# Kernel optimization log

Measured on AMD Instinct MI355X. Metric: run time of the kernel, lower is better.

## Reference

```python
import jax, jax.numpy as jnp
import numpy as np

B, D = 64, 1024
TAU = 1.0
NEG_SLOPE = 0.01  # torch LeakyReLU default


def setup_inputs() -> dict:
    key = jax.random.key(0)
    ks = jax.random.split(key, 7)
    lim = 1.0 / np.sqrt(D)
    return {
        "x": jax.random.normal(ks[0], (B, D), dtype=jnp.float32),
        "W1": jax.random.uniform(ks[1], (D, D), jnp.float32, -lim, lim),
        "b1": jax.random.uniform(ks[2], (D,), jnp.float32, -lim, lim),
        "W2": jax.random.uniform(ks[3], (D, D), jnp.float32, -lim, lim),
        "b2": jax.random.uniform(ks[4], (D,), jnp.float32, -lim, lim),
        "W3": jax.random.uniform(ks[5], (2, D), jnp.float32, -lim, lim),
        "b3": jax.random.uniform(ks[6], (2,), jnp.float32, -lim, lim),
    }


def _leaky(h):
    return jnp.where(h >= 0, h, NEG_SLOPE * h)


def _neural_sort(scores):
    # scores: [B, D]
    d = scores.shape[1]
    s = scores[..., None]                                  # [B, D, 1]
    A = jnp.abs(s - jnp.swapaxes(s, 1, 2))                 # [B, D, D] pairwise |s_i - s_j|
    # A @ (ones @ ones^T) == row-sum of A broadcast over columns
    Bsum = jnp.sum(A, axis=-1, keepdims=True)              # [B, D, 1]
    scaling = (d - 1 - 2 * jnp.arange(d)).astype(scores.dtype)  # (d+1-2*(i+1))
    C = s * scaling[None, None, :]                         # [B, D, D]
    P_max = jnp.swapaxes(C - Bsum, 1, 2)                   # [B, D, D]
    return jax.nn.softmax(P_max / TAU, axis=-1)


def reference(x, W1, b1, W2, b2, W3, b3):
    P_hat = _neural_sort(x)                                # [B, D, D]
    xs = jnp.einsum("bij,bj->bi", P_hat, x)                # soft-sorted x
    h = _leaky(xs @ W1.T + b1)
    h = _leaky(h @ W2.T + b2)
    return h @ W3.T + b3                                   # [B, 2]
```

## Files before the change

kernel.cpp:

```cpp
#include <hip/hip_runtime.h>
#include <math.h>

constexpr int Bn = 64;
constexpr int Dn = 1024;
constexpr float LOG2E = 1.4426950408889634f;
constexpr float LN2   = 0.6931471805599453f;

__device__ __forceinline__ float exp2_fast(float v) {
#if defined(__has_builtin)
#if __has_builtin(__builtin_amdgcn_exp2f)
  return __builtin_amdgcn_exp2f(v);
#else
  return exp2f(v);
#endif
#else
  return exp2f(v);
#endif
}

__global__ __launch_bounds__(512) void k0_sort_bsum(
    const float* __restrict__ x, float2* __restrict__ pairs_s,
    float4* __restrict__ desc, float* __restrict__ out) {
  int b    = blockIdx.x >> 1;
  int half = blockIdx.x & 1;
  int tid = threadIdx.x;
  __shared__ float xs_[Dn];
  __shared__ float cs_[Dn];
  __shared__ int   bkt_[Dn];
  __shared__ int   cnt[64], base_[64], off_[64];
  __shared__ float Ssum[64], cN[64], cS[64];
  if (tid < 64) { cnt[tid] = 0; off_[tid] = 0; Ssum[tid] = 0.f; }
  __syncthreads();
  float2 v2 = *(const float2*)(x + b * Dn + tid * 2);
  float xv[2] = {v2.x, v2.y};
  int bk[2];
#pragma unroll
  for (int u = 0; u < 2; ++u) {
    float z = exp2_fast(-2.455532f * xv[u]);
    float p = 1.f / (1.f + z);
    int t = (int)(p * 64.f);
    bk[u] = t < 0 ? 0 : (t > 63 ? 63 : t);
    atomicAdd(&cnt[bk[u]], 1);
    atomicAdd(&Ssum[bk[u]], xv[u]);
  }
  __syncthreads();
  if (tid < 64) {
    int c = cnt[tid]; int si = c;
    float fs = Ssum[tid]; float ss = fs;
#pragma unroll
    for (int d = 1; d < 64; d <<= 1) {
      int oi = __shfl_up(si, d, 64);
      float os = __shfl_up(ss, d, 64);
      if (tid >= d) { si += oi; ss += os; }
    }
    base_[tid] = si - c;
    float Stot = __shfl(ss, 63, 64);
    float Slo = ss - fs;
    cN[tid] = (float)(2 * (si - c) + c - Dn);
    cS[tid] = Stot - 2.f * Slo - fs;
  }
  __syncthreads();
#pragma unroll
  for (int u = 0; u < 2; ++u) {
    int pos = base_[bk[u]] + atomicAdd(&off_[bk[u]], 1);
    xs_[pos] = xv[u];
    bkt_[pos] = bk[u];
  }
  __syncthreads();
  {
    int p = half * 512 + tid;
    float xp = xs_[p];
    int q = bkt_[p];
    int lo = base_[q], hi = lo + cnt[q];
    float local = 0.f;
    for (int k = lo; k < hi; ++k) local += fabsf(xp - xs_[k]);
    float Bs = fmaf(xp, cN[q], cS[q]) + local;
    float c = -Bs * LOG2E;
    cs_[p] = c;
    pairs_s[b * Dn + p] = make_float2(xp * LOG2E, c);
  }
  __syncthreads();
  if (tid < 64) {
    int g = half * 64 + tid;
    int base = g * 8;
    float xlo = xs_[base], xhi = xlo;
    int ilo = base, ihi = base;
#pragma unroll
    for (int k = 1; k < 8; ++k) {
      float xx = xs_[base + k];
      if (xx < xlo) { xlo = xx; ilo = base + k; }
      if (xx > xhi) { xhi = xx; ihi = base + k; }
    }
    desc[b * 128 + g] =
        make_float4(xlo * LOG2E, cs_[ilo], xhi * LOG2E, cs_[ihi]);
  }
  if (b == 0 && half == 0 && tid < 128) out[tid] = 0.f;
}

__global__ __launch_bounds__(256, 4) void k2_softsort(
    const float2* __restrict__ pairs_s, const float4* __restrict__ desc,
    float* __restrict__ xs_out) {
  __shared__ float redM[4][64], redE[4][64], redD[4][64];
  int b  = blockIdx.x >> 4;
  int rc = blockIdx.x & 15;
  int tid = threadIdx.x;
  int w = tid >> 6, lane = tid & 63;
  int i = rc * 64 + lane;
  float sc = (float)(Dn - 1 - 2 * i);
  const float2* ps = pairs_s + b * Dn;
  const float4* dp = desc + b * 128;

  float gm[32];
  float m = -3.4e38f;
#pragma unroll 8
  for (int q = 0; q < 32; ++q) {
    float4 d = dp[q * 4 + w];
    float t0 = fmaf(sc, d.x, d.y);
    float t1 = fmaf(sc, d.z, d.w);
    float g = fmaxf(t0, t1);
    gm[q] = g;
    m = fmaxf(m, g);
  }
  redM[w][lane] = m;
  __syncthreads();
  float M = fmaxf(fmaxf(redM[0][lane], redM[1][lane]),
                  fmaxf(redM[2][lane], redM[3][lane]));
  float thresh = M - 32.f;

  float se = 0.f, sd = 0.f;
#pragma unroll 4
  for (int q = 0; q < 32; ++q) {
    if (__any(gm[q] > thresh)) {
      int base = (q * 4 + w) * 8;
#pragma unroll
      for (int u = 0; u < 8; ++u) {
        float2 v = ps[base + u];
        float e = exp2_fast(fmaf(sc, v.x, v.y - M));
        se += e;
        sd = fmaf(e, v.x, sd);
      }
    }
  }
  redE[w][lane] = se;
  redD[w][lane] = sd;
  __syncthreads();
  if (tid < 64) {
    float SE = (redE[0][lane] + redE[1][lane]) + (redE[2][lane] + redE[3][lane]);
    float SD = (redD[0][lane] + redD[1][lane]) + (redD[2][lane] + redD[3][lane]);
    xs_out[b * Dn + rc * 64 + lane] = SD / SE * LN2;
  }
}

template <bool TAIL>
__global__ __launch_bounds__(256) void layer_kernel(
    const float* __restrict__ in, const float* __restrict__ W,
    const float* __restrict__ bias, float* __restrict__ out,
    const float* __restrict__ W3, const float* __restrict__ b3,
    float* __restrict__ out2) {
  __shared__ float s[8][Dn + 4];
  __shared__ float red[8][8][16];
  __shared__ float r2[8][8][2];
  int xcd = blockIdx.x & 7;
  int idx = blockIdx.x >> 3;
  int nc = xcd * 16 + (idx & 15);
  int bc = idx >> 4;
  int tid = threadIdx.x;
  const float* src = in + bc * 8 * Dn;
#pragma unroll
  for (int u = 0; u < 8; ++u) {
    int idx2 = (u * 256 + tid) << 2;
    *(float4*)&s[idx2 >> 10][idx2 & 1023] = *(const float4*)(src + idx2);
  }
  __syncthreads();

  int bl = tid & 7;
  int nq = (tid >> 3) & 1;
  int kc = tid >> 4;
  int n0 = nc * 8 + nq * 4;
  const float* a  = &s[bl][kc * 64];
  const float* w0 = W + (size_t)(n0 + 0) * Dn + kc * 64;
  const float* w1 = W + (size_t)(n0 + 1) * Dn + kc * 64;
  const float* w2 = W + (size_t)(n0 + 2) * Dn + kc * 64;
  const float* w3 = W + (size_t)(n0 + 3) * Dn + kc * 64;
  float a0 = 0.f, a1 = 0.f, a2 = 0.f, a3 = 0.f;
#pragma unroll 4
  for (int kq = 0; kq < 16; ++kq) {
    float4 av = *(const float4*)(a + kq * 4);
    float4 b0 = *(const float4*)(w0 + kq * 4);
    float4 b1 = *(const float4*)(w1 + kq * 4);
    float4 b2 = *(const float4*)(w2 + kq * 4);
    float4 b3v = *(const float4*)(w3 + kq * 4);
    a0 = fmaf(av.x, b0.x, fmaf(av.y, b0.y, fmaf(av.z, b0.z, fmaf(av.w, b0.w, a0))));
    a1 = fmaf(av.x, b1.x, fmaf(av.y, b1.y, fmaf(av.z, b1.z, fmaf(av.w, b1.w, a1))));
    a2 = fmaf(av.x, b2.x, fmaf(av.y, b2.y, fmaf(av.z, b2.z, fmaf(av.w, b2.w, a2))));
    a3 = fmaf(av.x, b3v.x, fmaf(av.y, b3v.y, fmaf(av.z, b3v.z, fmaf(av.w, b3v.w, a3))));
  }
  red[bl][nq * 4 + 0][kc] = a0;
  red[bl][nq * 4 + 1][kc] = a1;
  red[bl][nq * 4 + 2][kc] = a2;
  red[bl][nq * 4 + 3][kc] = a3;
  __syncthreads();

  if (!TAIL) {
    if (tid < 64) {
      int bl2 = tid >> 3, nl2 = tid & 7;
      int n2 = nc * 8 + nl2;
      float hs = 0.f;
#pragma unroll
      for (int q = 0; q < 16; ++q) hs += red[bl2][nl2][q];
      float h = hs + bias[n2];
      h = h >= 0.f ? h : 0.01f * h;
      out[(bc * 8 + bl2) * Dn + n2] = h;
    }
  } else {
    if (tid < 64) {
      int bl2 = tid >> 3, nl2 = tid & 7;
      int n2 = nc * 8 + nl2;
      float hs = 0.f;
#pragma unroll
      for (int q = 0; q < 16; ++q) hs += red[bl2][nl2][q];
      float h = hs + bias[n2];
      h = h >= 0.f ? h : 0.01f * h;
      r2[bl2][nl2][0] = h * W3[n2];
      r2[bl2][nl2][1] = h * W3[Dn + n2];
    }
    __syncthreads();
    if (tid < 16) {
      int bl2 = tid >> 1, o = tid & 1;
      float t = 0.f;
#pragma unroll
      for (int q = 0; q < 8; ++q) t += r2[bl2][q][o];
      if (nc == 0) t += b3[o];
      atomicAdd(out2 + (bc * 8 + bl2) * 2 + o, t);
    }
  }
}

extern "C" void kernel_launch(void* const* d_in, const int* in_sizes, int n_in,
                              void* d_out, int out_size, void* d_ws, size_t ws_size,
                              hipStream_t stream) {
  const float* x  = (const float*)d_in[0];
  const float* W1 = (const float*)d_in[1];
  const float* b1 = (const float*)d_in[2];
  const float* W2 = (const float*)d_in[3];
  const float* b2 = (const float*)d_in[4];
  const float* W3 = (const float*)d_in[5];
  const float* b3 = (const float*)d_in[6];
  float* out = (float*)d_out;
  float* ws = (float*)d_ws;

  float2* pairs_s = (float2*)ws;
  float4* desc    = (float4*)(pairs_s + Bn * Dn);
  float*  xs      = (float*)(desc + Bn * 128);
  float*  h1      = xs + Bn * Dn;

  k0_sort_bsum<<<Bn * 2, 512, 0, stream>>>(x, pairs_s, desc, out);
  k2_softsort<<<Bn * 16, 256, 0, stream>>>(pairs_s, desc, xs);
  layer_kernel<false><<<1024, 256, 0, stream>>>(xs, W1, b1, h1,
                                                nullptr, nullptr, nullptr);
  layer_kernel<true><<<1024, 256, 0, stream>>>(h1, W2, b2, nullptr,
                                               W3, b3, out);
}
```

Before: 110.1 us.

## Fuse bucket sort into softsort kernel with redundant per-block recompute

Merges the bucket-sort/row-sum kernel into the soft-sort kernel. Each of the 16 blocks per batch row now recomputes the sort, pair values and group descriptors into shared memory instead of reading them from global workspace. This removes one kernel launch and the global round trip for pairs and descriptors. In exchange it repeats the sort work 16 times per row and uses more shared memory per block, which may lower occupancy.

Result: no change. 109.8 us (-0.2%).

```diff
diff --git a/kernel.cpp b/kernel.cpp
--- a/kernel.cpp
+++ b/kernel.cpp
@@ -18,24 +18,30 @@
 #endif
 }
 
-__global__ __launch_bounds__(512) void k0_sort_bsum(
-    const float* __restrict__ x, float2* __restrict__ pairs_s,
-    float4* __restrict__ desc, float* __restrict__ out) {
-  int b    = blockIdx.x >> 1;
-  int half = blockIdx.x & 1;
-  int tid = threadIdx.x;
-  __shared__ float xs_[Dn];
-  __shared__ float cs_[Dn];
-  __shared__ int   bkt_[Dn];
+__global__ __launch_bounds__(256) void k_sortsoft(
+    const float* __restrict__ x, float* __restrict__ xs_out,
+    float* __restrict__ out) {
+  __shared__ float  xs_[Dn];
+  __shared__ float2 prs_[Dn];
+  __shared__ int    bkt_[Dn];
+  __shared__ float4 desc_[128];
   __shared__ int   cnt[64], base_[64], off_[64];
   __shared__ float Ssum[64], cN[64], cS[64];
+  __shared__ float redM[4][64], redE[4][64], redD[4][64];
+
+  int b   = blockIdx.x >> 4;
+  int rc  = blockIdx.x & 15;
+  int tid = threadIdx.x;
+
   if (tid < 64) { cnt[tid] = 0; off_[tid] = 0; Ssum[tid] = 0.f; }
-  __syncthreads();
-  float2 v2 = *(const float2*)(x + b * Dn + tid * 2);
-  float xv[2] = {v2.x, v2.y};
-  int bk[2];
-#pragma unroll
-  for (int u = 0; u < 2; ++u) {
+  if (blockIdx.x == 0 && tid < 128) out[tid] = 0.f;
+  __syncthreads();
+
+  float4 v4 = *(const float4*)(x + b * Dn + tid * 4);
+  float xv[4] = {v4.x, v4.y, v4.z, v4.w};
+  int bk[4];
+#pragma unroll
+  for (int u = 0; u < 4; ++u) {
     float z = exp2_fast(-2.455532f * xv[u]);
     float p = 1.f / (1.f + z);
     int t = (int)(p * 64.f);
@@ -44,6 +50,7 @@
     atomicAdd(&Ssum[bk[u]], xv[u]);
   }
   __syncthreads();
+
   if (tid < 64) {
     int c = cnt[tid]; int si = c;
     float fs = Ssum[tid]; float ss = fs;
@@ -60,29 +67,30 @@
     cS[tid] = Stot - 2.f * Slo - fs;
   }
   __syncthreads();
-#pragma unroll
-  for (int u = 0; u < 2; ++u) {
+
+#pragma unroll
+  for (int u = 0; u < 4; ++u) {
     int pos = base_[bk[u]] + atomicAdd(&off_[bk[u]], 1);
     xs_[pos] = xv[u];
     bkt_[pos] = bk[u];
   }
   __syncthreads();
-  {
-    int p = half * 512 + tid;
+
+#pragma unroll
+  for (int r = 0; r < 4; ++r) {
+    int p = r * 256 + tid;
     float xp = xs_[p];
     int q = bkt_[p];
     int lo = base_[q], hi = lo + cnt[q];
     float local = 0.f;
     for (int k = lo; k < hi; ++k) local += fabsf(xp - xs_[k]);
     float Bs = fmaf(xp, cN[q], cS[q]) + local;
-    float c = -Bs * LOG2E;
-    cs_[p] = c;
-    pairs_s[b * Dn + p] = make_float2(xp * LOG2E, c);
-  }
-  __syncthreads();
-  if (tid < 64) {
-    int g = half * 64 + tid;
-    int base = g * 8;
+    prs_[p] = make_float2(xp * LOG2E, -Bs * LOG2E);
+  }
+  __syncthreads();
+
+  if (tid < 128) {
+    int base = tid * 8;
     float xlo = xs_[base], xhi = xlo;
     int ilo = base, ihi = base;
 #pragma unroll
@@ -91,30 +99,19 @@
       if (xx < xlo) { xlo = xx; ilo = base + k; }
       if (xx > xhi) { xhi = xx; ihi = base + k; }
     }
-    desc[b * 128 + g] =
-        make_float4(xlo * LOG2E, cs_[ilo], xhi * LOG2E, cs_[ihi]);
-  }
-  if (b == 0 && half == 0 && tid < 128) out[tid] = 0.f;
-}
-
-__global__ __launch_bounds__(256, 4) void k2_softsort(
-    const float2* __restrict__ pairs_s, const float4* __restrict__ desc,
-    float* __restrict__ xs_out) {
-  __shared__ float redM[4][64], redE[4][64], redD[4][64];
-  int b  = blockIdx.x >> 4;
-  int rc = blockIdx.x & 15;
-  int tid = threadIdx.x;
+    float2 plo = prs_[ilo], phi = prs_[ihi];
+    desc_[tid] = make_float4(plo.x, plo.y, phi.x, phi.y);
+  }
+  __syncthreads();
+
   int w = tid >> 6, lane = tid & 63;
   int i = rc * 64 + lane;
   float sc = (float)(Dn - 1 - 2 * i);
-  const float2* ps = pairs_s + b * Dn;
-  const float4* dp = desc + b * 128;
-
   float gm[32];
   float m = -3.4e38f;
 #pragma unroll 8
   for (int q = 0; q < 32; ++q) {
-    float4 d = dp[q * 4 + w];
+    float4 d = desc_[q * 4 + w];
     float t0 = fmaf(sc, d.x, d.y);
     float t1 = fmaf(sc, d.z, d.w);
     float g = fmaxf(t0, t1);
@@ -134,7 +131,7 @@
       int base = (q * 4 + w) * 8;
 #pragma unroll
       for (int u = 0; u < 8; ++u) {
-        float2 v = ps[base + u];
+        float2 v = prs_[base + u];
         float e = exp2_fast(fmaf(sc, v.x, v.y - M));
         se += e;
         sd = fmaf(e, v.x, sd);
@@ -249,13 +246,10 @@
   float* out = (float*)d_out;
   float* ws = (float*)d_ws;
 
-  float2* pairs_s = (float2*)ws;
-  float4* desc    = (float4*)(pairs_s + Bn * Dn);
-  float*  xs      = (float*)(desc + Bn * 128);
-  float*  h1      = xs + Bn * Dn;
-
-  k0_sort_bsum<<<Bn * 2, 512, 0, stream>>>(x, pairs_s, desc, out);
-  k2_softsort<<<Bn * 16, 256, 0, stream>>>(pairs_s, desc, xs);
+  float* xs = ws;
+  float* h1 = xs + Bn * Dn;
+
+  k_sortsoft<<<Bn * 16, 256, 0, stream>>>(x, xs, out);
   layer_kernel<false><<<1024, 256, 0, stream>>>(xs, W1, b1, h1,
                                                 nullptr, nullptr, nullptr);
   layer_kernel<true><<<1024, 256, 0, stream>>>(h1, W2, b2, nullptr,
```
